# Performance work log

Measured on AMD Instinct MI355X. Metric: run time of the kernel, lower is better.

## Reference

```python
import jax, jax.numpy as jnp
import numpy as np

EMBED = 8      # embed_dim == n_qubits == d_k (forced by reshapes in the source)
FFN = 2048
LN_EPS = 1e-5


def _layernorm(x, g, b):
    mu = jnp.mean(x, axis=-1, keepdims=True)
    var = jnp.mean(jnp.square(x - mu), axis=-1, keepdims=True)
    return (x - mu) * jax.lax.rsqrt(var + LN_EPS) * g + b


def _quantum_measure(theta):
    # RX(theta_i) on each wire of |0..0>, CNOT ladder 0->1->...->n-1,
    # then <Z_i>. Closed form: <Z_i> = prod_{j<=i} cos(theta_j).
    return jnp.cumprod(jnp.cos(theta), axis=-1)


def setup_inputs() -> dict:
    key = jax.random.key(0)
    ks = jax.random.split(key, 8)
    B, S = 32, 4096
    s_e = 1.0 / np.sqrt(EMBED)
    s_f = 1.0 / np.sqrt(FFN)
    return {
        "x": jax.random.normal(ks[0], (B, S, EMBED), jnp.float32),
        "Wq": jax.random.uniform(ks[1], (EMBED, EMBED), jnp.float32, -s_e, s_e),
        "Wo": jax.random.uniform(ks[2], (EMBED, EMBED), jnp.float32, -s_e, s_e),
        "W1": jax.random.uniform(ks[3], (FFN, EMBED), jnp.float32, -s_e, s_e),
        "b1": jax.random.uniform(ks[4], (FFN,), jnp.float32, -s_e, s_e),
        "W2": jax.random.uniform(ks[5], (EMBED, FFN), jnp.float32, -s_f, s_f),
        "b2": jax.random.uniform(ks[6], (EMBED,), jnp.float32, -s_f, s_f),
        "g1": jnp.ones((EMBED,), jnp.float32),
        "beta1": jnp.zeros((EMBED,), jnp.float32),
        "g2": jnp.ones((EMBED,), jnp.float32),
        "beta2": jnp.zeros((EMBED,), jnp.float32),
    }


def reference(x, Wq, Wo, W1, b1, W2, b2, g1, beta1, g2, beta2):
    # Quantum multi-head attention (num_heads=1, d_k=n_wires=8).
    # Note: k_proj / v_proj outputs are unused in the original forward.
    q = jnp.einsum("bse,fe->bsf", x, Wq)          # (B,S,E)
    attn = jnp.einsum("bse,fe->bsf", _quantum_measure(q), Wo)
    h = _layernorm(x + attn, g1, beta1)           # dropout is identity (eval)
    # Quantum feed-forward: measure -> linear1 -> relu -> linear2
    m = _quantum_measure(h)                       # (B,S,E)
    hid = jax.nn.relu(jnp.einsum("bse,fe->bsf", m, W1) + b1)  # (B,S,FFN)
    ffn = jnp.einsum("bsf,ef->bse", hid, W2) + b2
    return _layernorm(h + ffn, g2, beta2)
```

## Files before the change

### kernel.cpp

```cpp
#include <hip/hip_runtime.h>
#include <hip/hip_bf16.h>

#define FFN 2048
#define LN_EPS 1e-5f

typedef __attribute__((ext_vector_type(8))) short bf16x8;
typedef __attribute__((ext_vector_type(4))) float f32x4;

union FragU { bf16x8 v; unsigned u[4]; uint4 q; };

static __device__ __forceinline__ unsigned cvtpk(float lo, float hi) {
    unsigned r;
    asm("v_cvt_pk_bf16_f32 %0, %1, %2" : "=v"(r) : "v"(lo), "v"(hi));
    return r;
}

static __device__ __forceinline__ unsigned cvtpk_abs(float lo, float hi) {
    unsigned r;
    asm("v_cvt_pk_bf16_f32 %0, |%1|, |%2|" : "=v"(r) : "v"(lo), "v"(hi));
    return r;
}

static __device__ __forceinline__ ushort to_bf16(float f) {
    unsigned u = __float_as_uint(f);
    u += 0x7fffu + ((u >> 16) & 1u);
    return (ushort)(u >> 16);
}

static __device__ __forceinline__ float frombf(ushort u) {
    return __uint_as_float((unsigned)u << 16);
}

__global__ __launch_bounds__(256) void tbq_prep(
    const float* __restrict__ W1, const float* __restrict__ b1,
    const float* __restrict__ W2, uint4* __restrict__ ws)
{
    const int idx = blockIdx.x * 256 + threadIdx.x;
    if (idx >= 6336) return;
    ushort v[8] = {0,0,0,0,0,0,0,0};
    if (idx < 4224) {
        const int rec = idx / 33, r = idx % 33;
        if (r) {
            const int l32 = r - 1, c = l32 & 15, g = l32 >> 4;
            const int s = rec & 1, cc = rec >> 1;
            const int f = cc * 32 + s * 16 + c;
            if (g == 0) {
                #pragma unroll
                for (int j = 0; j < 8; ++j) v[j] = to_bf16(W1[f * 8 + j]);
            } else {
                v[0] = to_bf16(b1[f]);
            }
        }
    } else {
        const int i2 = idx - 4224;
        const int rec = i2 / 33, r = i2 % 33;
        if (r) {
            const int l32 = r - 1, g = l32 >> 3, c = l32 & 7, cc = rec;
            #pragma unroll
            for (int j = 0; j < 8; ++j) {
                const int fl = 4 * g + (j & 3) + 16 * (j >> 2);
                v[j] = to_bf16(0.5f * W2[c * FFN + cc * 32 + fl]);
            }
        }
    }
    union { ushort s[8]; uint4 q; } pk;
    #pragma unroll
    for (int j = 0; j < 8; ++j) pk.s[j] = v[j];
    ws[idx] = pk.q;
}

__global__ __launch_bounds__(256) void tbq_prepM(
    const float* __restrict__ W1, const float* __restrict__ b1,
    const float* __restrict__ W2, float* __restrict__ M)
{
    const int w = blockIdx.x * 4 + (threadIdx.x >> 6);
    const int lane = threadIdx.x & 63;
    const int e = w / 9, k = w % 9;
    float acc = 0.0f;
    #pragma unroll 4
    for (int i = 0; i < 32; ++i) {
        const int f = lane + i * 64;
        const float w2v = frombf(to_bf16(0.5f * W2[e * FFN + f]));
        const float ov  = (k < 8) ? frombf(to_bf16(W1[f * 8 + k]))
                                  : frombf(to_bf16(b1[f]));
        acc += w2v * ov;
    }
    #pragma unroll
    for (int m = 32; m >= 1; m >>= 1) acc += __shfl_xor(acc, m, 64);
    if (lane == 0) M[w] = acc;
}

__global__ __launch_bounds__(256) void tbq_mfma(
    const float* __restrict__ x,
    const float* __restrict__ Wq,
    const float* __restrict__ Wo,
    const float* __restrict__ b2,
    const float* __restrict__ g1,
    const float* __restrict__ beta1,
    const float* __restrict__ g2,
    const float* __restrict__ beta2,
    const uint4* __restrict__ ws,
    const float* __restrict__ M,
    float* __restrict__ out)
{
    __shared__ __align__(16) uint4 mS[128];
    __shared__ __align__(16) float part[4][128][8];

    const int tid  = threadIdx.x;
    const int lane = tid & 63;
    const int wv   = tid >> 6;
    const int c    = lane & 15;
    const int g    = lane >> 4;
    const int tok0 = blockIdx.x * 128;

    const int o1 = (lane < 32) ? (1 + lane) : 0;
    const int o2 = ((lane & 8) == 0) ? (1 + ((lane >> 4) << 3) + (lane & 7)) : 0;
    const int cc0 = wv * 16;

    FragU F0[4], F1[4], A2[4];
    #pragma unroll
    for (int p = 0; p < 3; ++p) {
        const int cc = cc0 + p;
        F0[p].q = (ws + cc * 66)[o1];
        F1[p].q = (ws + cc * 66 + 33)[o1];
        A2[p].q = (ws + 4224 + cc * 33)[o2];
    }

    float h[8];
    float m[8];
    if (tid < 128) {
        const int t = tok0 + tid;
        const float4* xr = (const float4*)(x + (size_t)t * 8);
        float4 xa = xr[0], xb = xr[1];
        float xv[8] = {xa.x, xa.y, xa.z, xa.w, xb.x, xb.y, xb.z, xb.w};

        float qm[8];
        {
            float cp = 1.0f;
            #pragma unroll
            for (int f = 0; f < 8; ++f) {
                float acc = 0.0f;
                #pragma unroll
                for (int e = 0; e < 8; ++e) acc += xv[e] * Wq[f * 8 + e];
                cp *= __cosf(acc);
                qm[f] = cp;
            }
        }
        float mu = 0.0f;
        #pragma unroll
        for (int f = 0; f < 8; ++f) {
            float acc = 0.0f;
            #pragma unroll
            for (int e = 0; e < 8; ++e) acc += qm[e] * Wo[f * 8 + e];
            h[f] = xv[f] + acc;
            mu += h[f];
        }
        mu *= 0.125f;
        float var = 0.0f;
        #pragma unroll
        for (int i = 0; i < 8; ++i) { float d = h[i] - mu; var += d * d; }
        var *= 0.125f;
        float rs = rsqrtf(var + LN_EPS);
        #pragma unroll
        for (int i = 0; i < 8; ++i) h[i] = (h[i] - mu) * rs * g1[i] + beta1[i];

        {
            float cp = 1.0f;
            #pragma unroll
            for (int i = 0; i < 8; ++i) { cp *= __cosf(h[i]); m[i] = cp; }
        }
        uint4 mq;
        mq.x = cvtpk(m[0], m[1]); mq.y = cvtpk(m[2], m[3]);
        mq.z = cvtpk(m[4], m[5]); mq.w = cvtpk(m[6], m[7]);
        mS[tid] = mq;
    }
    __syncthreads();

    FragU B1[8];
    #pragma unroll
    for (int T = 0; T < 8; ++T) {
        uint4 mr = mS[T * 16 + c];
        B1[T].u[0] = (g == 0) ? mr.x : ((g == 1) ? 0x00003F80u : 0u);
        B1[T].u[1] = (g == 0) ? mr.y : 0u;
        B1[T].u[2] = (g == 0) ? mr.z : 0u;
        B1[T].u[3] = (g == 0) ? mr.w : 0u;
    }

    f32x4 z4 = {0.f, 0.f, 0.f, 0.f};
    asm volatile("" : "+v"(z4));

    f32x4 acc[8] = {{0,0,0,0},{0,0,0,0},{0,0,0,0},{0,0,0,0},
                    {0,0,0,0},{0,0,0,0},{0,0,0,0},{0,0,0,0}};

    #pragma unroll
    for (int i = 0; i < 16; ++i) {
        const int cur = i & 3;
        if (i + 3 < 16) {
            const int nslot = (i + 3) & 3;
            const int cc = cc0 + i + 3;
            F0[nslot].q = (ws + cc * 66)[o1];
            F1[nslot].q = (ws + cc * 66 + 33)[o1];
            A2[nslot].q = (ws + 4224 + cc * 33)[o2];
        }
        __builtin_amdgcn_s_setprio(1);
        #pragma unroll
        for (int T = 0; T < 8; ++T) {
            f32x4 c0 = __builtin_amdgcn_mfma_f32_16x16x32_bf16(F0[cur].v, B1[T].v, z4, 0, 0, 0);
            f32x4 c1 = __builtin_amdgcn_mfma_f32_16x16x32_bf16(F1[cur].v, B1[T].v, z4, 0, 0, 0);
            FragU B2;
            B2.u[0] = cvtpk_abs(c0[0], c0[1]);
            B2.u[1] = cvtpk_abs(c0[2], c0[3]);
            B2.u[2] = cvtpk_abs(c1[0], c1[1]);
            B2.u[3] = cvtpk_abs(c1[2], c1[3]);
            acc[T] = __builtin_amdgcn_mfma_f32_16x16x32_bf16(A2[cur].v, B2.v, acc[T], 0, 0, 0);
        }
        __builtin_amdgcn_s_setprio(0);
    }

    if (g < 2) {
        #pragma unroll
        for (int T = 0; T < 8; ++T) {
            *(f32x4*)&part[wv][T * 16 + c][4 * g] = acc[T];
        }
    }
    __syncthreads();

    if (tid < 128) {
        float mb[9];
        #pragma unroll
        for (int k = 0; k < 8; ++k) mb[k] = frombf(to_bf16(m[k]));
        mb[8] = 1.0f;

        float ffnv[8];
        #pragma unroll
        for (int e = 0; e < 8; ++e) {
            float s = part[0][tid][e] + part[1][tid][e]
                    + part[2][tid][e] + part[3][tid][e];
            float lin = 0.0f;
            #pragma unroll
            for (int k = 0; k < 9; ++k) lin += M[e * 9 + k] * mb[k];
            ffnv[e] = s + lin;
        }

        float o[8];
        float mu2 = 0.0f;
        #pragma unroll
        for (int i = 0; i < 8; ++i) { o[i] = h[i] + ffnv[i] + b2[i]; mu2 += o[i]; }
        mu2 *= 0.125f;
        float v2 = 0.0f;
        #pragma unroll
        for (int i = 0; i < 8; ++i) { float d = o[i] - mu2; v2 += d * d; }
        v2 *= 0.125f;
        float rs2 = rsqrtf(v2 + LN_EPS);

        float res[8];
        #pragma unroll
        for (int i = 0; i < 8; ++i) res[i] = (o[i] - mu2) * rs2 * g2[i] + beta2[i];

        float4* orow = (float4*)(out + (size_t)(tok0 + tid) * 8);
        orow[0] = make_float4(res[0], res[1], res[2], res[3]);
        orow[1] = make_float4(res[4], res[5], res[6], res[7]);
    }
}

extern "C" void kernel_launch(void* const* d_in, const int* in_sizes, int n_in,
                              void* d_out, int out_size, void* d_ws, size_t ws_size,
                              hipStream_t stream) {
    const float* x     = (const float*)d_in[0];
    const float* Wq    = (const float*)d_in[1];
    const float* Wo    = (const float*)d_in[2];
    const float* W1    = (const float*)d_in[3];
    const float* b1    = (const float*)d_in[4];
    const float* W2    = (const float*)d_in[5];
    const float* b2    = (const float*)d_in[6];
    const float* g1    = (const float*)d_in[7];
    const float* beta1 = (const float*)d_in[8];
    const float* g2    = (const float*)d_in[9];
    const float* beta2 = (const float*)d_in[10];
    float* out = (float*)d_out;
    uint4* ws = (uint4*)d_ws;
    float* M  = (float*)(ws + 6336);

    tbq_prep<<<25, 256, 0, stream>>>(W1, b1, W2, ws);
    tbq_prepM<<<18, 256, 0, stream>>>(W1, b1, W2, M);

    const int ntok = in_sizes[0] / 8;
    const int grid = ntok / 128;
    tbq_mfma<<<grid, 256, 0, stream>>>(x, Wq, Wo, b2, g1, beta1, g2, beta2, ws, M, out);
}
```

Before: 40.09 us.

## Use 16x16x16 MFMA for first FFN layer with hand-scheduled inline asm, merge prep kernels

The first FFN matmul has K=9 (8 weights plus a bias term), so it now uses 16x16x16 bf16 MFMAs with 4-element fragments instead of zero-padded 16x16x32 ones. The workspace layout for W1/b1 is rebuilt to match, and the bias ones-column moves to lane group 2. The inner MFMA-convert-MFMA chain is written as inline asm with fixed scratch registers and explicit s_nop hazard padding, alternating two register sets. The two prep kernels are merged into one launch. The cost is hard-coded VGPR clobbers and manual hazard timing, which may clash with compiler register allocation.

```diff
diff --git a/kernel.cpp b/kernel.cpp
--- a/kernel.cpp
+++ b/kernel.cpp
@@ -5,9 +5,11 @@
 #define LN_EPS 1e-5f
 
 typedef __attribute__((ext_vector_type(8))) short bf16x8;
+typedef __attribute__((ext_vector_type(4))) short bf16x4;
 typedef __attribute__((ext_vector_type(4))) float f32x4;
 
-union FragU { bf16x8 v; unsigned u[4]; uint4 q; };
+union FragU  { bf16x8 v; unsigned u[4]; uint4 q; };
+union Frag2U { bf16x4 v; unsigned u[2]; uint2 d; };
 
 static __device__ __forceinline__ unsigned cvtpk(float lo, float hi) {
     unsigned r;
@@ -15,80 +17,107 @@
     return r;
 }
 
-static __device__ __forceinline__ unsigned cvtpk_abs(float lo, float hi) {
-    unsigned r;
-    asm("v_cvt_pk_bf16_f32 %0, |%1|, |%2|" : "=v"(r) : "v"(lo), "v"(hi));
-    return r;
-}
-
 static __device__ __forceinline__ ushort to_bf16(float f) {
     unsigned u = __float_as_uint(f);
     u += 0x7fffu + ((u >> 16) & 1u);
     return (ushort)(u >> 16);
 }
-
 static __device__ __forceinline__ float frombf(ushort u) {
     return __uint_as_float((unsigned)u << 16);
+}
+static __device__ __forceinline__ unsigned pk2u(ushort a, ushort b) {
+    return (unsigned)a | ((unsigned)b << 16);
 }
 
 __global__ __launch_bounds__(256) void tbq_prep(
     const float* __restrict__ W1, const float* __restrict__ b1,
     const float* __restrict__ W2, uint4* __restrict__ ws)
 {
-    const int idx = blockIdx.x * 256 + threadIdx.x;
-    if (idx >= 6336) return;
-    ushort v[8] = {0,0,0,0,0,0,0,0};
-    if (idx < 4224) {
-        const int rec = idx / 33, r = idx % 33;
-        if (r) {
-            const int l32 = r - 1, c = l32 & 15, g = l32 >> 4;
+    const int b = blockIdx.x;
+    if (b < 34) {
+        const int idx = b * 256 + threadIdx.x;
+        if (idx < 2112) {
+            const int rec = idx / 33, r = idx % 33;
+            ushort v[8] = {0,0,0,0,0,0,0,0};
+            if (r) {
+                const int l32 = r - 1, g = l32 >> 3, c = l32 & 7, cc = rec;
+                #pragma unroll
+                for (int j = 0; j < 8; ++j) {
+                    const int fl = 4 * g + (j & 3) + 16 * (j >> 2);
+                    v[j] = to_bf16(0.5f * W2[c * FFN + cc * 32 + fl]);
+                }
+            }
+            union { ushort s[8]; uint4 q; } pk;
+            #pragma unroll
+            for (int j = 0; j < 8; ++j) pk.s[j] = v[j];
+            ws[idx] = pk.q;
+        } else if (idx < 8512) {
+            const int i2 = idx - 2112;
+            const int rec = i2 / 50, r = i2 % 50;
             const int s = rec & 1, cc = rec >> 1;
-            const int f = cc * 32 + s * 16 + c;
-            if (g == 0) {
-                #pragma unroll
-                for (int j = 0; j < 8; ++j) v[j] = to_bf16(W1[f * 8 + j]);
-            } else {
-                v[0] = to_bf16(b1[f]);
+            uint2 val = make_uint2(0u, 0u);
+            if (r >= 1 && r <= 32) {
+                const int l32 = r - 1, c = l32 & 15, gg = l32 >> 4;
+                const int f = cc * 32 + s * 16 + c;
+                val.x = pk2u(to_bf16(W1[f * 8 + 4 * gg + 0]), to_bf16(W1[f * 8 + 4 * gg + 1]));
+                val.y = pk2u(to_bf16(W1[f * 8 + 4 * gg + 2]), to_bf16(W1[f * 8 + 4 * gg + 3]));
+            } else if (r >= 33 && r <= 48) {
+                const int c = r - 33;
+                const int f = cc * 32 + s * 16 + c;
+                val.x = pk2u(to_bf16(b1[f]), 0);
             }
+            ((uint2*)ws)[4224 + i2] = val;
         }
     } else {
-        const int i2 = idx - 4224;
-        const int rec = i2 / 33, r = i2 % 33;
-        if (r) {
-            const int l32 = r - 1, g = l32 >> 3, c = l32 & 7, cc = rec;
-            #pragma unroll
-            for (int j = 0; j < 8; ++j) {
-                const int fl = 4 * g + (j & 3) + 16 * (j >> 2);
-                v[j] = to_bf16(0.5f * W2[c * FFN + cc * 32 + fl]);
-            }
-        }
-    }
-    union { ushort s[8]; uint4 q; } pk;
-    #pragma unroll
-    for (int j = 0; j < 8; ++j) pk.s[j] = v[j];
-    ws[idx] = pk.q;
-}
-
-__global__ __launch_bounds__(256) void tbq_prepM(
-    const float* __restrict__ W1, const float* __restrict__ b1,
-    const float* __restrict__ W2, float* __restrict__ M)
-{
-    const int w = blockIdx.x * 4 + (threadIdx.x >> 6);
-    const int lane = threadIdx.x & 63;
-    const int e = w / 9, k = w % 9;
-    float acc = 0.0f;
-    #pragma unroll 4
-    for (int i = 0; i < 32; ++i) {
-        const int f = lane + i * 64;
-        const float w2v = frombf(to_bf16(0.5f * W2[e * FFN + f]));
-        const float ov  = (k < 8) ? frombf(to_bf16(W1[f * 8 + k]))
-                                  : frombf(to_bf16(b1[f]));
-        acc += w2v * ov;
-    }
-    #pragma unroll
-    for (int m = 32; m >= 1; m >>= 1) acc += __shfl_xor(acc, m, 64);
-    if (lane == 0) M[w] = acc;
-}
+        const int w = (b - 34) * 4 + (threadIdx.x >> 6);
+        const int lane = threadIdx.x & 63;
+        const int e = w / 9, k = w % 9;
+        float acc = 0.0f;
+        #pragma unroll 4
+        for (int i = 0; i < 32; ++i) {
+            const int f = lane + i * 64;
+            const float w2v = frombf(to_bf16(0.5f * W2[e * FFN + f]));
+            const float ov  = (k < 8) ? frombf(to_bf16(W1[f * 8 + k]))
+                                      : frombf(to_bf16(b1[f]));
+            acc += w2v * ov;
+        }
+        #pragma unroll
+        for (int m = 32; m >= 1; m >>= 1) acc += __shfl_xor(acc, m, 64);
+        if (lane == 0) ((float*)ws)[21248 + w] = acc;
+    }
+}
+
+#define TB_A(ACC, F0V, F1V, A2V, B1V)                                                  \
+    asm volatile(                                                                      \
+        "v_mfma_f32_16x16x16_bf16 v[40:43], %[f0], %[b1], %[z]\n\t"                    \
+        "v_mfma_f32_16x16x16_bf16 v[44:47], %[f1], %[b1], %[z]\n\t"                    \
+        "s_nop 7\n\t"                                                                  \
+        "s_nop 7\n\t"                                                                  \
+        "v_cvt_pk_bf16_f32 v48, |v40|, |v41|\n\t"                                      \
+        "v_cvt_pk_bf16_f32 v49, |v42|, |v43|\n\t"                                      \
+        "v_cvt_pk_bf16_f32 v50, |v44|, |v45|\n\t"                                      \
+        "v_cvt_pk_bf16_f32 v51, |v46|, |v47|\n\t"                                      \
+        "s_nop 3\n\t"                                                                  \
+        "v_mfma_f32_16x16x32_bf16 %[acc], %[a2], v[48:51], %[acc]"                     \
+        : [acc] "+v"(ACC)                                                              \
+        : [f0] "v"(F0V), [f1] "v"(F1V), [a2] "v"(A2V), [b1] "v"(B1V), [z] "v"(z4)      \
+        : "v40","v41","v42","v43","v44","v45","v46","v47","v48","v49","v50","v51")
+
+#define TB_B(ACC, F0V, F1V, A2V, B1V)                                                  \
+    asm volatile(                                                                      \
+        "v_mfma_f32_16x16x16_bf16 v[52:55], %[f0], %[b1], %[z]\n\t"                    \
+        "v_mfma_f32_16x16x16_bf16 v[56:59], %[f1], %[b1], %[z]\n\t"                    \
+        "s_nop 7\n\t"                                                                  \
+        "s_nop 7\n\t"                                                                  \
+        "v_cvt_pk_bf16_f32 v60, |v52|, |v53|\n\t"                                      \
+        "v_cvt_pk_bf16_f32 v61, |v54|, |v55|\n\t"                                      \
+        "v_cvt_pk_bf16_f32 v62, |v56|, |v57|\n\t"                                      \
+        "v_cvt_pk_bf16_f32 v63, |v58|, |v59|\n\t"                                      \
+        "s_nop 3\n\t"                                                                  \
+        "v_mfma_f32_16x16x32_bf16 %[acc], %[a2], v[60:63], %[acc]"                     \
+        : [acc] "+v"(ACC)                                                              \
+        : [f0] "v"(F0V), [f1] "v"(F1V), [a2] "v"(A2V), [b1] "v"(B1V), [z] "v"(z4)      \
+        : "v52","v53","v54","v55","v56","v57","v58","v59","v60","v61","v62","v63")
 
 __global__ __launch_bounds__(256) void tbq_mfma(
     const float* __restrict__ x,
@@ -100,7 +129,6 @@
     const float* __restrict__ g2,
     const float* __restrict__ beta2,
     const uint4* __restrict__ ws,
-    const float* __restrict__ M,
     float* __restrict__ out)
 {
     __shared__ __align__(16) uint4 mS[128];
@@ -113,21 +141,24 @@
     const int g    = lane >> 4;
     const int tok0 = blockIdx.x * 128;
 
-    const int o1 = (lane < 32) ? (1 + lane) : 0;
-    const int o2 = ((lane & 8) == 0) ? (1 + ((lane >> 4) << 3) + (lane & 7)) : 0;
+    const uint2* ws2 = (const uint2*)ws;
+    const float* M   = (const float*)ws + 21248;
+
+    const int o1x = (g < 2) ? (1 + c + 16 * g) : ((g == 2) ? (33 + c) : 0);
+    const int o2  = ((lane & 8) == 0) ? (1 + ((lane >> 4) << 3) + (lane & 7)) : 0;
     const int cc0 = wv * 16;
 
-    FragU F0[4], F1[4], A2[4];
+    Frag2U F0[4], F1[4];
+    FragU  A2[4];
     #pragma unroll
     for (int p = 0; p < 3; ++p) {
         const int cc = cc0 + p;
-        F0[p].q = (ws + cc * 66)[o1];
-        F1[p].q = (ws + cc * 66 + 33)[o1];
-        A2[p].q = (ws + 4224 + cc * 33)[o2];
-    }
-
-    float h[8];
-    float m[8];
+        F0[p].d = ws2[4224 + (cc * 2 + 0) * 50 + o1x];
+        F1[p].d = ws2[4224 + (cc * 2 + 1) * 50 + o1x];
+        A2[p].q = (ws + cc * 33)[o2];
+    }
+
+    float h[8], m[8];
     if (tid < 128) {
         const int t = tok0 + tid;
         const float4* xr = (const float4*)(x + (size_t)t * 8);
@@ -176,14 +207,14 @@
     }
     __syncthreads();
 
-    FragU B1[8];
+    Frag2U B1[8];
     #pragma unroll
     for (int T = 0; T < 8; ++T) {
         uint4 mr = mS[T * 16 + c];
-        B1[T].u[0] = (g == 0) ? mr.x : ((g == 1) ? 0x00003F80u : 0u);
-        B1[T].u[1] = (g == 0) ? mr.y : 0u;
-        B1[T].u[2] = (g == 0) ? mr.z : 0u;
-        B1[T].u[3] = (g == 0) ? mr.w : 0u;
+        unsigned u0 = (g == 0) ? mr.x : ((g == 1) ? mr.z : ((g == 2) ? 0x00003F80u : 0u));
+        unsigned u1 = (g == 0) ? mr.y : ((g == 1) ? mr.w : 0u);
+        B1[T].u[0] = u0;
+        B1[T].u[1] = u1;
     }
 
     f32x4 z4 = {0.f, 0.f, 0.f, 0.f};
@@ -191,31 +222,30 @@
 
     f32x4 acc[8] = {{0,0,0,0},{0,0,0,0},{0,0,0,0},{0,0,0,0},
                     {0,0,0,0},{0,0,0,0},{0,0,0,0},{0,0,0,0}};
+    asm volatile("s_nop 3" ::: "memory");
 
     #pragma unroll
     for (int i = 0; i < 16; ++i) {
         const int cur = i & 3;
         if (i + 3 < 16) {
-            const int nslot = (i + 3) & 3;
+            const int ns = (i + 3) & 3;
             const int cc = cc0 + i + 3;
-            F0[nslot].q = (ws + cc * 66)[o1];
-            F1[nslot].q = (ws + cc * 66 + 33)[o1];
-            A2[nslot].q = (ws + 4224 + cc * 33)[o2];
+            F0[ns].d = ws2[4224 + (cc * 2 + 0) * 50 + o1x];
+            F1[ns].d = ws2[4224 + (cc * 2 + 1) * 50 + o1x];
+            A2[ns].q = (ws + cc * 33)[o2];
         }
         __builtin_amdgcn_s_setprio(1);
-        #pragma unroll
-        for (int T = 0; T < 8; ++T) {
-            f32x4 c0 = __builtin_amdgcn_mfma_f32_16x16x32_bf16(F0[cur].v, B1[T].v, z4, 0, 0, 0);
-            f32x4 c1 = __builtin_amdgcn_mfma_f32_16x16x32_bf16(F1[cur].v, B1[T].v, z4, 0, 0, 0);
-            FragU B2;
-            B2.u[0] = cvtpk_abs(c0[0], c0[1]);
-            B2.u[1] = cvtpk_abs(c0[2], c0[3]);
-            B2.u[2] = cvtpk_abs(c1[0], c1[1]);
-            B2.u[3] = cvtpk_abs(c1[2], c1[3]);
-            acc[T] = __builtin_amdgcn_mfma_f32_16x16x32_bf16(A2[cur].v, B2.v, acc[T], 0, 0, 0);
-        }
+        TB_A(acc[0], F0[cur].v, F1[cur].v, A2[cur].v, B1[0].v);
+        TB_B(acc[1], F0[cur].v, F1[cur].v, A2[cur].v, B1[1].v);
+        TB_A(acc[2], F0[cur].v, F1[cur].v, A2[cur].v, B1[2].v);
+        TB_B(acc[3], F0[cur].v, F1[cur].v, A2[cur].v, B1[3].v);
+        TB_A(acc[4], F0[cur].v, F1[cur].v, A2[cur].v, B1[4].v);
+        TB_B(acc[5], F0[cur].v, F1[cur].v, A2[cur].v, B1[5].v);
+        TB_A(acc[6], F0[cur].v, F1[cur].v, A2[cur].v, B1[6].v);
+        TB_B(acc[7], F0[cur].v, F1[cur].v, A2[cur].v, B1[7].v);
         __builtin_amdgcn_s_setprio(0);
     }
+    asm volatile("s_nop 7\n\ts_nop 7" ::: "memory");
 
     if (g < 2) {
         #pragma unroll
@@ -279,12 +309,10 @@
     const float* beta2 = (const float*)d_in[10];
     float* out = (float*)d_out;
     uint4* ws = (uint4*)d_ws;
-    float* M  = (float*)(ws + 6336);
-
-    tbq_prep<<<25, 256, 0, stream>>>(W1, b1, W2, ws);
-    tbq_prepM<<<18, 256, 0, stream>>>(W1, b1, W2, M);
+
+    tbq_prep<<<52, 256, 0, stream>>>(W1, b1, W2, ws);
 
     const int ntok = in_sizes[0] / 8;
     const int grid = ntok / 128;
-    tbq_mfma<<<grid, 256, 0, stream>>>(x, Wq, Wo, b2, g1, beta1, g2, beta2, ws, M, out);
-}
+    tbq_mfma<<<grid, 256, 0, stream>>>(x, Wq, Wo, b2, g1, beta1, g2, beta2, ws, out);
+}
```

New measurement: 34.95 us. 1.15x faster.
